# Performance work log

Measured on AMD Instinct MI355X. Metric: run time of the kernel, lower is better.

The kernel has to match this reference:

```python
import jax, jax.numpy as jnp
import numpy as np

EPS = 1e-5
C = 128
B = 16384
SYMBIOTIC = 4.0
NUM_PARENTS = 16
CHILDREN_PER_PARENT = 7


def _inverse(v):
    # torch: sort -> rank -> reversed rank -> gather sorted values
    idx0 = np.argsort(v, kind='stable')
    value = v[idx0]
    idx1 = np.argsort(idx0, kind='stable')  # ranks
    idx2 = v.shape[0] - 1 - idx1
    return value[idx2]


def _build_stats():
    counts = np.floor(50000.0 * 0.97 ** np.arange(C)) + 1.0  # long-tailed
    N = counts.sum()
    weight = (N / counts).astype(np.float32)
    prior = np.eye(C, dtype=np.float32)
    for p in range(NUM_PARENTS):
        ch = NUM_PARENTS + CHILDREN_PER_PARENT * p + np.arange(CHILDREN_PER_PARENT)
        prior[p, ch] = 1.0
    prior_me = (prior == 0).astype(np.float32)          # 1 - prior, keep only exact 1s
    prior_ms = prior - np.eye(C, dtype=np.float32)      # prior (0/1) minus eye
    v1_sig = np.log(N / counts - 1.0 + EPS).astype(np.float32)
    v2_sig = _inverse(v1_sig).astype(np.float32)
    v1_sm = np.log(counts / N + EPS).astype(np.float32)
    v2_sm = _inverse(v1_sm).astype(np.float32)
    return weight, prior_me, prior_ms, v1_sig, v2_sig, v1_sm, v2_sm


def setup_inputs() -> dict:
    key = jax.random.key(0)
    k1, k2 = jax.random.split(key)
    weight, prior_me, prior_ms, v1s, v2s, v1m, v2m = _build_stats()
    logits = 0.5 * jax.random.normal(k1, (12, B, C), dtype=jnp.float32)
    target = (jax.random.uniform(k2, (B, C)) < 0.1).astype(jnp.float32)
    return {
        'logits': logits, 'target': target,
        'weight': jnp.asarray(weight),
        'prior_me': jnp.asarray(prior_me), 'prior_ms': jnp.asarray(prior_ms),
        'v1_sigmoid': jnp.asarray(v1s), 'v2_sigmoid': jnp.asarray(v2s),
        'v1_softmax': jnp.asarray(v1m), 'v2_softmax': jnp.asarray(v2m),
    }


def reference(logits, target, weight, prior_me, prior_ms,
              v1_sigmoid, v2_sigmoid, v1_softmax, v2_softmax):
    zero = jnp.zeros_like(v1_sigmoid)
    # experts 0-5: sigmoid variants (long-tailed / balanced / inversed, twice)
    sig_shift = jnp.stack([zero, v1_sigmoid, v1_sigmoid - v2_sigmoid] * 2)  # [6,C]
    a_sig = jax.nn.sigmoid(logits[:6] - sig_shift[:, None, :])
    # experts 6-11: local-softmax variants
    sm_shift = jnp.stack([zero, v1_softmax, v1_softmax - v2_softmax] * 2)   # [6,C]
    e = jnp.exp(logits[6:] + sm_shift[:, None, :])                          # [6,B,C]
    denom = jnp.einsum('ebc,cd->ebd', e, prior_me) + e
    a_sm = e / (denom + EPS)
    acti = jnp.clip(jnp.concatenate([a_sig, a_sm], axis=0), EPS, 1.0 - EPS)  # [12,B,C]
    # weighted BCE per expert, summed
    bce = -weight * (target * jnp.log(acti) + (1.0 - target) * jnp.log(1.0 - acti))
    loss = jnp.sum(jnp.mean(bce, axis=(1, 2)))
    # symbiotic regularizer on experts 3,4,5,9,10,11
    row_sum = jnp.sum(prior_ms, axis=1)                 # [C]
    n_nz = jnp.sum(row_sum > 0).astype(acti.dtype)
    bsz = acti.shape[1]

    def symb(a):  # a: [B,C] activated logits
        def step(acc, xs):
            mask_row, parent = xs                       # [C], [B]
            term = jnp.log1p(jnp.exp(a - parent[:, None]))  # [B,C]
            rs = jnp.sum(mask_row)
            contrib = jnp.where(rs > 0, jnp.sum(term * mask_row) / (bsz * rs), 0.0)
            return acc + contrib, None
        total, _ = jax.lax.scan(step, jnp.float32(0.0), (prior_ms, a.T))
        return total / n_nz

    reg = jax.vmap(symb)(acti[jnp.array([3, 4, 5, 9, 10, 11])])
    return loss + SYMBIOTIC * jnp.sum(reg)
```

## Files before the change

kernel.cpp:

```cpp
#include <hip/hip_runtime.h>
#include <math.h>

#define CC 128
#define BB 16384
#define MEPS 1e-5f


__global__ __launch_bounds__(256) void mel_kernel(
    const float* __restrict__ logits, const float* __restrict__ target,
    const float* __restrict__ weight,
    const float* __restrict__ v1s, const float* __restrict__ v2s,
    const float* __restrict__ v1m, const float* __restrict__ v2m,
    float* __restrict__ out)
{
    const int lane = threadIdx.x & 63;
    const int wib  = threadIdx.x >> 6;
    const int wave_id   = blockIdx.x * (blockDim.x >> 6) + wib;
    const int num_waves = gridDim.x * (blockDim.x >> 6);

    const int c0 = lane * 2;
    const int c1 = c0 + 1;

    const float w0 = weight[c0], w1 = weight[c1];
    const float a1s0 = v1s[c0], a1s1 = v1s[c1];
    const float a2s0 = v2s[c0], a2s1 = v2s[c1];
    const float a1m0 = v1m[c0], a1m1 = v1m[c1];
    const float a2m0 = v2m[c0], a2m1 = v2m[c1];

    const float sshift0[3] = {0.f, a1s0, a1s0 - a2s0};
    const float sshift1[3] = {0.f, a1s1, a1s1 - a2s1};
    const float mshift0[3] = {0.f, a1m0, a1m0 - a2m0};
    const float mshift1[3] = {0.f, a1m1, a1m1 - a2m1};

    const bool child0 = (c0 >= 16);
    const bool child1 = (c1 >= 16);
    const int p0 = child0 ? (c0 - 16) / 7 : 0;
    const int p1 = child1 ? (c1 - 16) / 7 : 0;
    const int p0lane = p0 >> 1, p0sel = p0 & 1;
    const int p1lane = p1 >> 1, p1sel = p1 & 1;

    float acc_bce  = 0.f;
    float acc_symb = 0.f;

    for (int b = wave_id; b < BB; b += num_waves) {
        const size_t rowoff = (size_t)b * CC + c0;
        const float2 t2 = *(const float2*)(target + rowoff);
        const bool t0 = (t2.x > 0.5f);
        const bool t1 = (t2.y > 0.5f);

        #pragma unroll
        for (int e = 0; e < 6; ++e) {
            const float2 x = *(const float2*)(logits + (size_t)e * ((size_t)BB * CC) + rowoff);
            const int si = e % 3;
            float a0 = 1.f / (1.f + __expf(sshift0[si] - x.x));
            float a1 = 1.f / (1.f + __expf(sshift1[si] - x.y));
            a0 = fminf(fmaxf(a0, MEPS), 1.f - MEPS);
            a1 = fminf(fmaxf(a1, MEPS), 1.f - MEPS);
            acc_bce += w0 * (t0 ? __logf(a0) : __logf(1.f - a0));
            acc_bce += w1 * (t1 ? __logf(a1) : __logf(1.f - a1));
            if (e >= 3) {
                const float sa0 = __shfl(a0, p0lane, 64);
                const float sb0 = __shfl(a1, p0lane, 64);
                const float ap0 = p0sel ? sb0 : sa0;
                const float sa1 = __shfl(a0, p1lane, 64);
                const float sb1 = __shfl(a1, p1lane, 64);
                const float ap1 = p1sel ? sb1 : sa1;
                if (child0) acc_symb += __logf(1.f + __expf(a0 - ap0));
                if (child1) acc_symb += __logf(1.f + __expf(a1 - ap1));
            }
        }

        #pragma unroll
        for (int j = 0; j < 6; ++j) {
            const float2 x = *(const float2*)(logits + (size_t)(6 + j) * ((size_t)BB * CC) + rowoff);
            const int si = j % 3;
            const float e0 = __expf(x.x + mshift0[si]);
            const float e1 = __expf(x.y + mshift1[si]);
            float s = e0 + e1;
            #pragma unroll
            for (int off = 32; off > 0; off >>= 1)
                s += __shfl_xor(s, off, 64);
            const float pa0 = __shfl(e0, p0lane, 64);
            const float pb0 = __shfl(e1, p0lane, 64);
            const float ep0 = p0sel ? pb0 : pa0;
            const float pa1 = __shfl(e0, p1lane, 64);
            const float pb1 = __shfl(e1, p1lane, 64);
            const float ep1 = p1sel ? pb1 : pa1;

            const float den0 = s - (child0 ? ep0 : 0.f) + MEPS;
            const float den1 = s - (child1 ? ep1 : 0.f) + MEPS;
            float a0 = e0 / den0;
            float a1 = e1 / den1;
            a0 = fminf(fmaxf(a0, MEPS), 1.f - MEPS);
            a1 = fminf(fmaxf(a1, MEPS), 1.f - MEPS);
            acc_bce += w0 * (t0 ? __logf(a0) : __logf(1.f - a0));
            acc_bce += w1 * (t1 ? __logf(a1) : __logf(1.f - a1));
            if (j >= 3) {
                const float apden = s + MEPS;
                float ap0 = ep0 / apden;
                float ap1 = ep1 / apden;
                ap0 = fminf(fmaxf(ap0, MEPS), 1.f - MEPS);
                ap1 = fminf(fmaxf(ap1, MEPS), 1.f - MEPS);
                if (child0) acc_symb += __logf(1.f + __expf(a0 - ap0));
                if (child1) acc_symb += __logf(1.f + __expf(a1 - ap1));
            }
        }
    }

    float val = -acc_bce * (1.f / ((float)BB * (float)CC))
              + acc_symb * (4.f / (112.f * (float)BB));

    #pragma unroll
    for (int off = 32; off > 0; off >>= 1)
        val += __shfl_xor(val, off, 64);

    __shared__ float sdata[4];
    if (lane == 0) sdata[wib] = val;
    __syncthreads();
    if (threadIdx.x == 0) {
        float v = sdata[0] + sdata[1] + sdata[2] + sdata[3];
        atomicAdd(out, v);
    }
}

extern "C" void kernel_launch(void* const* d_in, const int* in_sizes, int n_in,
                              void* d_out, int out_size, void* d_ws, size_t ws_size,
                              hipStream_t stream) {
    const float* logits = (const float*)d_in[0];
    const float* target = (const float*)d_in[1];
    const float* weight = (const float*)d_in[2];
    const float* v1s = (const float*)d_in[5];
    const float* v2s = (const float*)d_in[6];
    const float* v1m = (const float*)d_in[7];
    const float* v2m = (const float*)d_in[8];
    float* out = (float*)d_out;

    hipMemsetAsync(out, 0, sizeof(float), stream);

    const int block = 256;
    const int grid  = 2048;
    mel_kernel<<<grid, block, 0, stream>>>(logits, target, weight,
                                           v1s, v2s, v1m, v2m, out);
}
```

Before: 183.6 us.

## Preload all rows upfront, use log-sigmoid BCE, rcp math, two-pass reduction

```diff
diff --git a/kernel.cpp b/kernel.cpp
--- a/kernel.cpp
+++ b/kernel.cpp
@@ -4,105 +4,126 @@
 #define CC 128
 #define BB 16384
 #define MEPS 1e-5f
+#define LEPS  (-11.512925464970229f)
+#define L1ME  (-1.0000050000287824e-05f)
+#define NBLK 2048
 
 
-__global__ __launch_bounds__(256) void mel_kernel(
+__global__ __launch_bounds__(256) void mel_main(
     const float* __restrict__ logits, const float* __restrict__ target,
     const float* __restrict__ weight,
     const float* __restrict__ v1s, const float* __restrict__ v2s,
     const float* __restrict__ v1m, const float* __restrict__ v2m,
-    float* __restrict__ out)
+    float* __restrict__ partial)
 {
     const int lane = threadIdx.x & 63;
     const int wib  = threadIdx.x >> 6;
-    const int wave_id   = blockIdx.x * (blockDim.x >> 6) + wib;
-    const int num_waves = gridDim.x * (blockDim.x >> 6);
+    const int wave = blockIdx.x * 4 + wib;
+    const int b0   = wave * 2;
 
     const int c0 = lane * 2;
     const int c1 = c0 + 1;
 
     const float w0 = weight[c0], w1 = weight[c1];
-    const float a1s0 = v1s[c0], a1s1 = v1s[c1];
-    const float a2s0 = v2s[c0], a2s1 = v2s[c1];
-    const float a1m0 = v1m[c0], a1m1 = v1m[c1];
-    const float a2m0 = v2m[c0], a2m1 = v2m[c1];
+    const float s1a = v1s[c0], s1b = v1s[c1];
+    const float s2a = v2s[c0], s2b = v2s[c1];
+    const float m1a = v1m[c0], m1b = v1m[c1];
+    const float m2a = v2m[c0], m2b = v2m[c1];
 
-    const float sshift0[3] = {0.f, a1s0, a1s0 - a2s0};
-    const float sshift1[3] = {0.f, a1s1, a1s1 - a2s1};
-    const float mshift0[3] = {0.f, a1m0, a1m0 - a2m0};
-    const float mshift1[3] = {0.f, a1m1, a1m1 - a2m1};
+    const float sshift0[3] = {0.f, s1a, s1a - s2a};
+    const float sshift1[3] = {0.f, s1b, s1b - s2b};
+    const float mshift0[3] = {0.f, m1a, m1a - m2a};
+    const float mshift1[3] = {0.f, m1b, m1b - m2b};
 
-    const bool child0 = (c0 >= 16);
-    const bool child1 = (c1 >= 16);
-    const int p0 = child0 ? (c0 - 16) / 7 : 0;
-    const int p1 = child1 ? (c1 - 16) / 7 : 0;
-    const int p0lane = p0 >> 1, p0sel = p0 & 1;
-    const int p1lane = p1 >> 1, p1sel = p1 & 1;
+    const float childf = (lane >= 8) ? 1.f : 0.f;
+    const int p0 = (c0 >= 16) ? (c0 - 16) / 7 : 0;
+    const int p1 = (c1 >= 16) ? (c1 - 16) / 7 : 0;
+    const int p0lane = p0 >> 1; const int p0sel = p0 & 1;
+    const int p1lane = p1 >> 1; const int p1sel = p1 & 1;
+
+    float2 tg[2], xs[6][2], xm[6][2];
+    #pragma unroll
+    for (int r = 0; r < 2; ++r) {
+        const size_t ro = (size_t)(b0 + r) * CC + c0;
+        tg[r] = *(const float2*)(target + ro);
+        #pragma unroll
+        for (int e = 0; e < 6; ++e)
+            xs[e][r] = *(const float2*)(logits + (size_t)e * ((size_t)BB * CC) + ro);
+        #pragma unroll
+        for (int j = 0; j < 6; ++j)
+            xm[j][r] = *(const float2*)(logits + (size_t)(6 + j) * ((size_t)BB * CC) + ro);
+    }
 
     float acc_bce  = 0.f;
     float acc_symb = 0.f;
 
-    for (int b = wave_id; b < BB; b += num_waves) {
-        const size_t rowoff = (size_t)b * CC + c0;
-        const float2 t2 = *(const float2*)(target + rowoff);
-        const bool t0 = (t2.x > 0.5f);
-        const bool t1 = (t2.y > 0.5f);
+    #pragma unroll
+    for (int r = 0; r < 2; ++r) {
+        const bool t0 = tg[r].x > 0.5f;
+        const bool t1 = tg[r].y > 0.5f;
 
         #pragma unroll
         for (int e = 0; e < 6; ++e) {
-            const float2 x = *(const float2*)(logits + (size_t)e * ((size_t)BB * CC) + rowoff);
             const int si = e % 3;
-            float a0 = 1.f / (1.f + __expf(sshift0[si] - x.x));
-            float a1 = 1.f / (1.f + __expf(sshift1[si] - x.y));
-            a0 = fminf(fmaxf(a0, MEPS), 1.f - MEPS);
-            a1 = fminf(fmaxf(a1, MEPS), 1.f - MEPS);
-            acc_bce += w0 * (t0 ? __logf(a0) : __logf(1.f - a0));
-            acc_bce += w1 * (t1 ? __logf(a1) : __logf(1.f - a1));
+            const float z0 = xs[e][r].x - sshift0[si];
+            const float z1 = xs[e][r].y - sshift1[si];
+            const float ex0 = __expf(-z0), ex1 = __expf(-z1);
+            const float sp0 = __logf(1.f + ex0), sp1 = __logf(1.f + ex1);
+            const float la0  = fminf(fmaxf(-sp0,      LEPS), L1ME);
+            const float l1a0 = fminf(fmaxf(-z0 - sp0, LEPS), L1ME);
+            const float la1  = fminf(fmaxf(-sp1,      LEPS), L1ME);
+            const float l1a1 = fminf(fmaxf(-z1 - sp1, LEPS), L1ME);
+            acc_bce += w0 * (t0 ? la0 : l1a0);
+            acc_bce += w1 * (t1 ? la1 : l1a1);
             if (e >= 3) {
-                const float sa0 = __shfl(a0, p0lane, 64);
-                const float sb0 = __shfl(a1, p0lane, 64);
-                const float ap0 = p0sel ? sb0 : sa0;
-                const float sa1 = __shfl(a0, p1lane, 64);
-                const float sb1 = __shfl(a1, p1lane, 64);
-                const float ap1 = p1sel ? sb1 : sa1;
-                if (child0) acc_symb += __logf(1.f + __expf(a0 - ap0));
-                if (child1) acc_symb += __logf(1.f + __expf(a1 - ap1));
+                const float a0 = __builtin_amdgcn_rcpf(1.f + ex0);
+                const float a1 = __builtin_amdgcn_rcpf(1.f + ex1);
+                const float ca0 = fminf(fmaxf(a0, MEPS), 1.f - MEPS);
+                const float ca1 = fminf(fmaxf(a1, MEPS), 1.f - MEPS);
+                const float qa0 = __shfl(ca0, p0lane, 64);
+                const float qb0 = __shfl(ca1, p0lane, 64);
+                const float cap0 = p0sel ? qb0 : qa0;
+                const float qa1 = __shfl(ca0, p1lane, 64);
+                const float qb1 = __shfl(ca1, p1lane, 64);
+                const float cap1 = p1sel ? qb1 : qa1;
+                acc_symb += childf * __logf(1.f + __expf(ca0 - cap0));
+                acc_symb += childf * __logf(1.f + __expf(ca1 - cap1));
             }
         }
 
         #pragma unroll
         for (int j = 0; j < 6; ++j) {
-            const float2 x = *(const float2*)(logits + (size_t)(6 + j) * ((size_t)BB * CC) + rowoff);
             const int si = j % 3;
-            const float e0 = __expf(x.x + mshift0[si]);
-            const float e1 = __expf(x.y + mshift1[si]);
-            float s = e0 + e1;
+            const float e0 = __expf(xm[j][r].x + mshift0[si]);
+            const float e1 = __expf(xm[j][r].y + mshift1[si]);
+            float S = e0 + e1;
             #pragma unroll
             for (int off = 32; off > 0; off >>= 1)
-                s += __shfl_xor(s, off, 64);
-            const float pa0 = __shfl(e0, p0lane, 64);
-            const float pb0 = __shfl(e1, p0lane, 64);
-            const float ep0 = p0sel ? pb0 : pa0;
-            const float pa1 = __shfl(e0, p1lane, 64);
-            const float pb1 = __shfl(e1, p1lane, 64);
-            const float ep1 = p1sel ? pb1 : pa1;
+                S += __shfl_xor(S, off, 64);
+            const float qa0 = __shfl(e0, p0lane, 64);
+            const float qb0 = __shfl(e1, p0lane, 64);
+            const float ep0 = p0sel ? qb0 : qa0;
+            const float qa1 = __shfl(e0, p1lane, 64);
+            const float qb1 = __shfl(e1, p1lane, 64);
+            const float ep1 = p1sel ? qb1 : qa1;
 
-            const float den0 = s - (child0 ? ep0 : 0.f) + MEPS;
-            const float den1 = s - (child1 ? ep1 : 0.f) + MEPS;
-            float a0 = e0 / den0;
-            float a1 = e1 / den1;
+            const float den0 = S + MEPS - childf * ep0;
+            const float den1 = S + MEPS - childf * ep1;
+            float a0 = e0 * __builtin_amdgcn_rcpf(den0);
+            float a1 = e1 * __builtin_amdgcn_rcpf(den1);
             a0 = fminf(fmaxf(a0, MEPS), 1.f - MEPS);
             a1 = fminf(fmaxf(a1, MEPS), 1.f - MEPS);
-            acc_bce += w0 * (t0 ? __logf(a0) : __logf(1.f - a0));
-            acc_bce += w1 * (t1 ? __logf(a1) : __logf(1.f - a1));
+            const float arg0 = t0 ? a0 : 1.f - a0;
+            const float arg1 = t1 ? a1 : 1.f - a1;
+            acc_bce += w0 * __logf(arg0);
+            acc_bce += w1 * __logf(arg1);
             if (j >= 3) {
-                const float apden = s + MEPS;
-                float ap0 = ep0 / apden;
-                float ap1 = ep1 / apden;
+                const float rS = __builtin_amdgcn_rcpf(S + MEPS);
+                float ap0 = ep0 * rS, ap1 = ep1 * rS;
                 ap0 = fminf(fmaxf(ap0, MEPS), 1.f - MEPS);
                 ap1 = fminf(fmaxf(ap1, MEPS), 1.f - MEPS);
-                if (child0) acc_symb += __logf(1.f + __expf(a0 - ap0));
-                if (child1) acc_symb += __logf(1.f + __expf(a1 - ap1));
+                acc_symb += childf * __logf(1.f + __expf(a0 - ap0));
+                acc_symb += childf * __logf(1.f + __expf(a1 - ap1));
             }
         }
     }
@@ -117,10 +138,25 @@
     __shared__ float sdata[4];
     if (lane == 0) sdata[wib] = val;
     __syncthreads();
-    if (threadIdx.x == 0) {
-        float v = sdata[0] + sdata[1] + sdata[2] + sdata[3];
-        atomicAdd(out, v);
-    }
+    if (threadIdx.x == 0)
+        partial[blockIdx.x] = sdata[0] + sdata[1] + sdata[2] + sdata[3];
+}
+
+__global__ __launch_bounds__(256) void mel_reduce(
+    const float* __restrict__ partial, float* __restrict__ out)
+{
+    float v = 0.f;
+    #pragma unroll
+    for (int i = 0; i < NBLK / 256; ++i)
+        v += partial[threadIdx.x + i * 256];
+    #pragma unroll
+    for (int off = 32; off > 0; off >>= 1)
+        v += __shfl_xor(v, off, 64);
+    __shared__ float s[4];
+    const int lane = threadIdx.x & 63, wib = threadIdx.x >> 6;
+    if (lane == 0) s[wib] = v;
+    __syncthreads();
+    if (threadIdx.x == 0) out[0] = s[0] + s[1] + s[2] + s[3];
 }
 
 extern "C" void kernel_launch(void* const* d_in, const int* in_sizes, int n_in,
@@ -133,12 +169,10 @@
     const float* v2s = (const float*)d_in[6];
     const float* v1m = (const float*)d_in[7];
     const float* v2m = (const float*)d_in[8];
+    float* partial = (float*)d_ws;
     float* out = (float*)d_out;
 
-    hipMemsetAsync(out, 0, sizeof(float), stream);
-
-    const int block = 256;
-    const int grid  = 2048;
-    mel_kernel<<<grid, block, 0, stream>>>(logits, target, weight,
-                                           v1s, v2s, v1m, v2m, out);
+    mel_main<<<NBLK, 256, 0, stream>>>(logits, target, weight,
+                                       v1s, v2s, v1m, v2m, partial);
+    mel_reduce<<<1, 256, 0, stream>>>(partial, out);
 }
```

Result: faster. 172.5 us (-6.1%).
